# Optimization experiments

Hardware: AMD Instinct MI355X
Metric: run time of the kernel (lower is better)

## Reference

```python
import jax, jax.numpy as jnp
import numpy as np

EMBED = 1024
HEADS = 16
HEAD_DIM = EMBED // HEADS
LN_EPS = 1e-5


def setup_inputs() -> dict:
    key = jax.random.key(0)
    ks = jax.random.split(key, 7)
    B, S = 2, 2048
    x = jax.random.normal(ks[0], (B, S, EMBED), dtype=jnp.float32)
    attn_params = jax.random.uniform(ks[1], (B, S, 3 * EMBED), dtype=jnp.float32)
    sc = 1.0 / np.sqrt(EMBED)
    Wqkv = jax.random.normal(ks[2], (3 * EMBED, EMBED), dtype=jnp.float32) * sc
    Wout = jax.random.normal(ks[3], (EMBED, EMBED), dtype=jnp.float32) * sc
    b_out = jnp.zeros((EMBED,), dtype=jnp.float32)
    gamma = jnp.ones((EMBED,), dtype=jnp.float32)
    beta = jnp.zeros((EMBED,), dtype=jnp.float32)
    return {"x": x, "attn_params": attn_params, "Wqkv": Wqkv, "Wout": Wout,
            "b_out": b_out, "gamma": gamma, "beta": beta}


def reference(x, attn_params, Wqkv, Wout, b_out, gamma, beta):
    B, S, E = x.shape
    # qkv projection (no bias) followed by elementwise attn_params scaling
    qkv = jnp.einsum('bse,fe->bsf', x, Wqkv) * attn_params  # [B,S,3E]
    q, k, v = jnp.split(qkv, 3, axis=-1)
    # [B,H,S,D]
    q = q.reshape(B, S, HEADS, HEAD_DIM).transpose(0, 2, 1, 3)
    k = k.reshape(B, S, HEADS, HEAD_DIM).transpose(0, 2, 1, 3)
    v = v.reshape(B, S, HEADS, HEAD_DIM).transpose(0, 2, 1, 3)
    scores = jnp.einsum('bhqd,bhkd->bhqk', q, k) / jnp.sqrt(jnp.float32(HEAD_DIM))
    attn = jax.nn.softmax(scores, axis=-1)
    weighted = jnp.einsum('bhqk,bhkd->bhqd', attn, v)  # [B,H,S,D]
    weighted = weighted.transpose(0, 2, 1, 3).reshape(B, S, E)
    out = jnp.einsum('bse,fe->bsf', weighted, Wout) + b_out
    out = out + x  # residual
    # layernorm over last dim
    mu = jnp.mean(out, axis=-1, keepdims=True)
    var = jnp.mean(jnp.square(out - mu), axis=-1, keepdims=True)
    return (out - mu) * jax.lax.rsqrt(var + LN_EPS) * gamma + beta
```

## Files before the change

### kernel.cpp

```cpp
#include <hip/hip_runtime.h>

typedef float f32x4 __attribute__((ext_vector_type(4)));
typedef short s16x8 __attribute__((ext_vector_type(8)));
typedef unsigned short u16;

#define AS1 __attribute__((address_space(1)))
#define AS3 __attribute__((address_space(3)))

__device__ __forceinline__ u16 f2bf(float f){
    union { float f; unsigned u; } v; v.f = f;
    unsigned r = v.u + 0x7FFFu + ((v.u >> 16) & 1u);
    return (u16)(r >> 16);
}

__device__ __forceinline__ void pswap(unsigned &A, unsigned &B){
    asm("v_permlane32_swap_b32 %0, %1\n\tv_permlane16_swap_b32 %0, %1" : "+v"(A), "+v"(B));
}
__device__ __forceinline__ unsigned cvtpk(float lo, float hi){
    unsigned w;
    asm("v_cvt_pk_bf16_f32 %0, %1, %2" : "=v"(w) : "v"(lo), "v"(hi));
    return w;
}

__global__ __launch_bounds__(256) void cvt3_bf16(
    const float* __restrict__ a, u16* __restrict__ da, int na,
    const float* __restrict__ b, u16* __restrict__ db, int nb,
    const float* __restrict__ c, u16* __restrict__ dc, int nc)
{
    int i = blockIdx.x * 256 + threadIdx.x;
    const float* s; u16* d; int off;
    if (i < na){ s = a; d = da; off = i; }
    else if (i < na + nb){ s = b; d = db; off = i - na; }
    else if (i < na + nb + nc){ s = c; d = dc; off = i - na - nb; }
    else return;
    float4 v = ((const float4*)s)[off];
    ushort4 o;
    o.x = f2bf(v.x); o.y = f2bf(v.y); o.z = f2bf(v.z); o.w = f2bf(v.w);
    ((ushort4*)d)[off] = o;
}

__global__ __launch_bounds__(256) void gemm128_qkv(
    const u16* __restrict__ A, const u16* __restrict__ Bw,
    int N, int K,
    const float* __restrict__ e0, u16* __restrict__ Cout)
{
    __shared__ u16 As[2][128 * 32];
    __shared__ u16 Bs[2][128 * 32];
    const int tid = threadIdx.x;
    const int w = tid >> 6, lane = tid & 63;
    const int g = lane >> 4, c = lane & 15;
    const int wr = w >> 1, wc = w & 1;

    const int bid = blockIdx.x;
    const int xcd = bid & 7, lin = bid >> 3;
    const int rowBase = (xcd * 4 + (lin & 3)) * 128;
    const int colBase = (lin >> 2) * 128;

    f32x4 acc[4][4] = {};

    auto STAGE = [&](int pb, int k0){
#pragma unroll
        for (int i = 0; i < 2; ++i){
            int o  = i * 4096 + tid * 16;
            int r  = o >> 6;
            int ce = (o & 63) >> 1;
            const u16* ga = A  + (size_t)(rowBase + r) * K + (k0 + ce);
            __builtin_amdgcn_global_load_lds((const AS1 void*)ga,
                (AS3 void*)((char*)As[pb] + i * 4096 + w * 1024), 16, 0, 0);
            const u16* gb = Bw + (size_t)(colBase + r) * K + (k0 + ce);
            __builtin_amdgcn_global_load_lds((const AS1 void*)gb,
                (AS3 void*)((char*)Bs[pb] + i * 4096 + w * 1024), 16, 0, 0);
        }
    };

    const int nt = K >> 5;
    STAGE(0, 0);
    __syncthreads();

    for (int t = 0; t < nt; ++t){
        const int cur = t & 1;
        if (t + 1 < nt) STAGE(cur ^ 1, (t + 1) * 32);

        s16x8 af[4], bfr[4];
#pragma unroll
        for (int m = 0; m < 4; ++m){
            int row = wr * 64 + m * 16 + c;
            af[m] = *(const s16x8*)((const char*)As[cur] + row * 64 + g * 16);
        }
#pragma unroll
        for (int n = 0; n < 4; ++n){
            int row = wc * 64 + n * 16 + c;
            bfr[n] = *(const s16x8*)((const char*)Bs[cur] + row * 64 + g * 16);
        }
#pragma unroll
        for (int m = 0; m < 4; ++m)
#pragma unroll
            for (int n = 0; n < 4; ++n)
                acc[m][n] = __builtin_amdgcn_mfma_f32_16x16x32_bf16(af[m], bfr[n], acc[m][n], 0, 0, 0);
        __syncthreads();
    }

#pragma unroll
    for (int m = 0; m < 4; ++m){
        const int rbase = rowBase + wr * 64 + m * 16 + g * 4;
        float ev[16];
#pragma unroll
        for (int n = 0; n < 4; ++n){
            const int cc = colBase + wc * 64 + n * 16 + c;
#pragma unroll
            for (int j = 0; j < 4; ++j)
                ev[n * 4 + j] = e0[(size_t)(rbase + j) * N + cc];
        }
#pragma unroll
        for (int n = 0; n < 4; ++n){
            const int cc = colBase + wc * 64 + n * 16 + c;
#pragma unroll
            for (int j = 0; j < 4; ++j){
                float apv = ev[n * 4 + j];
                if (cc < 1024) apv *= 0.18033688f;
                Cout[(size_t)(rbase + j) * N + cc] = f2bf(acc[m][n][j] * apv);
            }
        }
    }
}

__global__ __launch_bounds__(256) void gemm_bt(
    const u16* __restrict__ A, const u16* __restrict__ Bw,
    int M, int N, int K,
    const float* __restrict__ e0, const float* __restrict__ e1,
    float* __restrict__ Cout)
{
    __shared__ u16 As[2][128 * 32];
    __shared__ u16 Bs[2][128 * 32];
    const int tid = threadIdx.x;
    const int w = tid >> 6, lane = tid & 63;
    const int g = lane >> 4, c = lane & 15;
    const int wr = w >> 1, wc = w & 1;
    const int rowBase = blockIdx.y * 128;
    const int colBase = blockIdx.x * 128;

    f32x4 acc[4][4] = {};

    auto STAGE = [&](int pb, int k0){
#pragma unroll
        for (int i = 0; i < 2; ++i){
            int o  = i * 4096 + tid * 16;
            int r  = o >> 6;
            int ce = (o & 63) >> 1;
            const u16* ga = A  + (size_t)(rowBase + r) * K + (k0 + ce);
            __builtin_amdgcn_global_load_lds((const AS1 void*)ga,
                (AS3 void*)((char*)As[pb] + i * 4096 + w * 1024), 16, 0, 0);
            const u16* gb = Bw + (size_t)(colBase + r) * K + (k0 + ce);
            __builtin_amdgcn_global_load_lds((const AS1 void*)gb,
                (AS3 void*)((char*)Bs[pb] + i * 4096 + w * 1024), 16, 0, 0);
        }
    };

    const int nt = K >> 5;
    STAGE(0, 0);
    __syncthreads();

    for (int t = 0; t < nt; ++t){
        const int cur = t & 1;
        if (t + 1 < nt) STAGE(cur ^ 1, (t + 1) * 32);

        s16x8 af[4], bfr[4];
#pragma unroll
        for (int m = 0; m < 4; ++m){
            int row = wr * 64 + m * 16 + c;
            af[m] = *(const s16x8*)((const char*)As[cur] + row * 64 + g * 16);
        }
#pragma unroll
        for (int n = 0; n < 4; ++n){
            int row = wc * 64 + n * 16 + c;
            bfr[n] = *(const s16x8*)((const char*)Bs[cur] + row * 64 + g * 16);
        }
#pragma unroll
        for (int m = 0; m < 4; ++m)
#pragma unroll
            for (int n = 0; n < 4; ++n)
                acc[m][n] = __builtin_amdgcn_mfma_f32_16x16x32_bf16(af[m], bfr[n], acc[m][n], 0, 0, 0);
        __syncthreads();
    }

    float bcol[4];
#pragma unroll
    for (int n = 0; n < 4; ++n)
        bcol[n] = e0[colBase + wc * 64 + n * 16 + c];

#pragma unroll
    for (int m = 0; m < 4; ++m){
        const int rbase = rowBase + wr * 64 + m * 16 + g * 4;
        float ev[16];
#pragma unroll
        for (int n = 0; n < 4; ++n){
            const int cc = colBase + wc * 64 + n * 16 + c;
#pragma unroll
            for (int j = 0; j < 4; ++j)
                ev[n * 4 + j] = e1[(size_t)(rbase + j) * N + cc];
        }
#pragma unroll
        for (int n = 0; n < 4; ++n){
            const int cc = colBase + wc * 64 + n * 16 + c;
#pragma unroll
            for (int j = 0; j < 4; ++j)
                Cout[(size_t)(rbase + j) * N + cc] = acc[m][n][j] + bcol[n] + ev[n * 4 + j];
        }
    }
}

__global__ __launch_bounds__(256) void vtrans(const u16* __restrict__ qkv, u16* __restrict__ vt){
    __shared__ u16 t_[64 * 64];
    int bh = blockIdx.x; int b = bh >> 4; int h = bh & 15;
    int st = blockIdx.y;
    int tid = threadIdx.x;
#pragma unroll
    for (int i = 0; i < 2; ++i){
        int id = i * 256 + tid;
        int sr = id >> 3, c8 = id & 7;
        uint4 v = *(const uint4*)(qkv + (size_t)(b * 2048 + st * 64 + sr) * 3072 + 2048 + h * 64 + c8 * 8);
        *(uint4*)((char*)t_ + ((sr * 128 + c8 * 16) ^ ((sr & 7) << 4))) = v;
    }
    __syncthreads();
#pragma unroll
    for (int i = 0; i < 2; ++i){
        int id = i * 256 + tid;
        int d = id >> 3, s8 = (id & 7) * 8;
        u16 tmp[8];
#pragma unroll
        for (int jj = 0; jj < 8; ++jj){
            int s = s8 + jj;
            tmp[jj] = *(const u16*)((const char*)t_ + ((s * 128 + d * 2) ^ ((s & 7) << 4)));
        }
        *(uint4*)(vt + ((size_t)bh * 64 + d) * 2048 + st * 64 + s8) = *(uint4*)tmp;
    }
}

__global__ __launch_bounds__(512) void attn_k(const u16* __restrict__ qkv,
                                              const u16* __restrict__ vt,
                                              u16* __restrict__ o)
{
    __shared__ u16 Kl[2][64 * 64];
    __shared__ u16 Vl[2][64 * 64];
    int bh = blockIdx.x; int b = bh >> 4, h = bh & 15;
    int qt = blockIdx.y;
    int tid = threadIdx.x;
    int w = tid >> 6, lane = tid & 63, g = lane >> 4, c = lane & 15;

    const size_t qrow = (size_t)(b * 2048 + qt * 128 + w * 16 + c);
    s16x8 qf[2];
    qf[0] = *(const s16x8*)(qkv + qrow * 3072 + h * 64 + g * 8);
    qf[1] = *(const s16x8*)(qkv + qrow * 3072 + h * 64 + 32 + g * 8);

    const s16x8 ones8 = {16256, 16256, 16256, 16256, 16256, 16256, 16256, 16256};

    f32x4 oa[4] = {};
    f32x4 la = {};

    int kr = tid >> 3, c8 = tid & 7;
    const u16* kg = qkv + (size_t)(b * 2048 + kr) * 3072 + 1024 + h * 64 + c8 * 8;
    const u16* vg = vt + ((size_t)bh * 64 + kr) * 2048 + c8 * 8;
    const int so = (kr * 128 + c8 * 16) ^ ((kr & 7) << 4);

    uint4 ks = *(const uint4*)kg;
    uint4 vs = *(const uint4*)vg;
    *(uint4*)((char*)Kl[0] + so) = ks;
    *(uint4*)((char*)Vl[0] + so) = vs;
    __syncthreads();

    for (int t = 0; t < 32; ++t){
        const int cur = t & 1;
        if (t < 31){
            ks = *(const uint4*)(kg + (size_t)(t + 1) * 64 * 3072);
            vs = *(const uint4*)(vg + (t + 1) * 64);
        }

        f32x4 st[4];
        __builtin_amdgcn_s_setprio(1);
#pragma unroll
        for (int kt = 0; kt < 4; ++kt){
            int row = kt * 16 + c;
            s16x8 kf0 = *(const s16x8*)((const char*)Kl[cur] + ((row * 128 + g * 16) ^ ((row & 7) << 4)));
            s16x8 kf1 = *(const s16x8*)((const char*)Kl[cur] + ((row * 128 + 64 + g * 16) ^ ((row & 7) << 4)));
            f32x4 a = {};
            a = __builtin_amdgcn_mfma_f32_16x16x32_bf16(kf0, qf[0], a, 0, 0, 0);
            a = __builtin_amdgcn_mfma_f32_16x16x32_bf16(kf1, qf[1], a, 0, 0, 0);
            st[kt] = a;
        }
        __builtin_amdgcn_s_setprio(0);

        unsigned W[4][2];
#pragma unroll
        for (int kt = 0; kt < 4; ++kt){
            float p0 = __builtin_amdgcn_exp2f(st[kt][0]);
            float p1 = __builtin_amdgcn_exp2f(st[kt][1]);
            float p2 = __builtin_amdgcn_exp2f(st[kt][2]);
            float p3 = __builtin_amdgcn_exp2f(st[kt][3]);
            W[kt][0] = cvtpk(p0, p1);
            W[kt][1] = cvtpk(p2, p3);
        }

        __builtin_amdgcn_s_setprio(1);
#pragma unroll
        for (int kb = 0; kb < 2; ++kb){
            unsigned t0 = W[kb * 2][0], t2 = W[kb * 2 + 1][0];
            pswap(t0, t2);
            unsigned t1 = W[kb * 2][1], t3 = W[kb * 2 + 1][1];
            pswap(t1, t3);
            union { unsigned u[4]; s16x8 v; } pu;
            pu.u[0] = t0; pu.u[1] = t1; pu.u[2] = t2; pu.u[3] = t3;
#pragma unroll
            for (int dt = 0; dt < 4; ++dt){
                int vrow = dt * 16 + c;
                s16x8 vf = *(const s16x8*)((const char*)Vl[cur] + ((vrow * 128 + kb * 64 + g * 16) ^ ((vrow & 7) << 4)));
                oa[dt] = __builtin_amdgcn_mfma_f32_16x16x32_bf16(vf, pu.v, oa[dt], 0, 0, 0);
            }
            la = __builtin_amdgcn_mfma_f32_16x16x32_bf16(ones8, pu.v, la, 0, 0, 0);
        }
        __builtin_amdgcn_s_setprio(0);

        if (t < 31){
            *(uint4*)((char*)Kl[cur ^ 1] + so) = ks;
            *(uint4*)((char*)Vl[cur ^ 1] + so) = vs;
        }
        __syncthreads();
    }

    float inv = 1.0f / la[0];
#pragma unroll
    for (int dt = 0; dt < 4; ++dt){
        u16 t4[4];
#pragma unroll
        for (int j = 0; j < 4; ++j) t4[j] = f2bf(oa[dt][j] * inv);
        *(uint2*)(o + qrow * 1024 + h * 64 + dt * 16 + g * 4) = *(uint2*)t4;
    }
}

__global__ __launch_bounds__(256) void ln_k(const float* __restrict__ tmp,
                                            const float* __restrict__ gamma,
                                            const float* __restrict__ beta,
                                            float* __restrict__ out)
{
    int row = blockIdx.x;
    int tid = threadIdx.x;
    float4 v = ((const float4*)(tmp + (size_t)row * 1024))[tid];
    float s  = v.x + v.y + v.z + v.w;
    float ss = v.x * v.x + v.y * v.y + v.z * v.z + v.w * v.w;
    for (int m = 1; m < 64; m <<= 1){ s += __shfl_xor(s, m); ss += __shfl_xor(ss, m); }
    __shared__ float red[8];
    int w = tid >> 6;
    if ((tid & 63) == 0){ red[w * 2] = s; red[w * 2 + 1] = ss; }
    __syncthreads();
    s  = red[0] + red[2] + red[4] + red[6];
    ss = red[1] + red[3] + red[5] + red[7];
    float mu  = s * (1.f / 1024.f);
    float var = ss * (1.f / 1024.f) - mu * mu;
    float inv = rsqrtf(var + 1e-5f);
    float4 g4 = ((const float4*)gamma)[tid];
    float4 b4 = ((const float4*)beta)[tid];
    float4 r;
    r.x = (v.x - mu) * inv * g4.x + b4.x;
    r.y = (v.y - mu) * inv * g4.y + b4.y;
    r.z = (v.z - mu) * inv * g4.z + b4.z;
    r.w = (v.w - mu) * inv * g4.w + b4.w;
    ((float4*)(out + (size_t)row * 1024))[tid] = r;
}

extern "C" void kernel_launch(void* const* d_in, const int* in_sizes, int n_in,
                              void* d_out, int out_size, void* d_ws, size_t ws_size,
                              hipStream_t stream)
{
    const float* x     = (const float*)d_in[0];
    const float* ap    = (const float*)d_in[1];
    const float* wqkv  = (const float*)d_in[2];
    const float* wout  = (const float*)d_in[3];
    const float* bout  = (const float*)d_in[4];
    const float* gamma = (const float*)d_in[5];
    const float* beta  = (const float*)d_in[6];
    float* out = (float*)d_out;

    char* ws = (char*)d_ws;
    u16* xb    = (u16*)ws;  ws += (size_t)4096 * 1024 * 2;
    u16* wqkvb = (u16*)ws;  ws += (size_t)3072 * 1024 * 2;
    u16* woutb = (u16*)ws;  ws += (size_t)1024 * 1024 * 2;
    u16* qkvb  = (u16*)ws;  ws += (size_t)4096 * 3072 * 2;
    u16* vtb   = (u16*)ws;  ws += (size_t)32 * 64 * 2048 * 2;
    u16* attnb = (u16*)ws;  ws += (size_t)4096 * 1024 * 2;
    float* tmp = (float*)ws;

    const int na = 4096 * 1024 / 4, nb = 3072 * 1024 / 4, nc = 1024 * 1024 / 4;
    cvt3_bf16<<<(na + nb + nc + 255) / 256, 256, 0, stream>>>(x, xb, na, wqkv, wqkvb, nb, wout, woutb, nc);

    gemm128_qkv<<<768, 256, 0, stream>>>(xb, wqkvb, 3072, 1024, ap, qkvb);
    vtrans<<<dim3(32, 32), 256, 0, stream>>>(qkvb, vtb);
    attn_k<<<dim3(32, 16), 512, 0, stream>>>(qkvb, vtb, attnb);
    gemm_bt<<<dim3(8, 32), 256, 0, stream>>>(attnb, woutb, 4096, 1024, 1024, bout, x, tmp);
    ln_k<<<4096, 256, 0, stream>>>(tmp, gamma, beta, out);
}
```

Before: 141.9 us.

## Double attention KV tile to 128 keys and drop XCD-aware QKV GEMM block mapping

The attention kernel now stages 128 keys per iteration instead of 64 into doubled LDS buffers, halving the number of loop iterations and barriers. Each iteration computes eight score tiles and four PV k-blocks. Separately, the QKV GEMM switches from an XCD-swizzled 1D block index to a plain 2D grid. This raises LDS use and register pressure in the attention kernel and may lose the L2 locality the XCD mapping provided.

Result: no change. 141.9 us (+0.0%).

```diff
diff --git a/kernel.cpp b/kernel.cpp
--- a/kernel.cpp
+++ b/kernel.cpp
@@ -39,7 +39,7 @@
     ((ushort4*)d)[off] = o;
 }
 
-__global__ __launch_bounds__(256) void gemm128_qkv(
+__global__ __launch_bounds__(256) void gemm_qkv(
     const u16* __restrict__ A, const u16* __restrict__ Bw,
     int N, int K,
     const float* __restrict__ e0, u16* __restrict__ Cout)
@@ -50,11 +50,8 @@
     const int w = tid >> 6, lane = tid & 63;
     const int g = lane >> 4, c = lane & 15;
     const int wr = w >> 1, wc = w & 1;
-
-    const int bid = blockIdx.x;
-    const int xcd = bid & 7, lin = bid >> 3;
-    const int rowBase = (xcd * 4 + (lin & 3)) * 128;
-    const int colBase = (lin >> 2) * 128;
+    const int rowBase = blockIdx.y * 128;
+    const int colBase = blockIdx.x * 128;
 
     f32x4 acc[4][4] = {};
 
@@ -240,8 +237,8 @@
                                               const u16* __restrict__ vt,
                                               u16* __restrict__ o)
 {
-    __shared__ u16 Kl[2][64 * 64];
-    __shared__ u16 Vl[2][64 * 64];
+    __shared__ u16 Kl[2][128 * 64];
+    __shared__ u16 Vl[2][64 * 128];
     int bh = blockIdx.x; int b = bh >> 4, h = bh & 15;
     int qt = blockIdx.y;
     int tid = threadIdx.x;
@@ -259,26 +256,36 @@
 
     int kr = tid >> 3, c8 = tid & 7;
     const u16* kg = qkv + (size_t)(b * 2048 + kr) * 3072 + 1024 + h * 64 + c8 * 8;
-    const u16* vg = vt + ((size_t)bh * 64 + kr) * 2048 + c8 * 8;
-    const int so = (kr * 128 + c8 * 16) ^ ((kr & 7) << 4);
-
-    uint4 ks = *(const uint4*)kg;
-    uint4 vs = *(const uint4*)vg;
-    *(uint4*)((char*)Kl[0] + so) = ks;
-    *(uint4*)((char*)Vl[0] + so) = vs;
+    const int sk0 = (kr * 128 + c8 * 16) ^ ((kr & 7) << 4);
+    const int sk1 = sk0 + 64 * 128;
+    int dr = tid >> 3;
+    const u16* vg = vt + ((size_t)bh * 64 + dr) * 2048 + c8 * 8;
+    const int sv0 = (dr * 256 + c8 * 16) ^ ((dr & 7) << 4);
+    const int sv1 = sv0 + 128;
+
+    uint4 ks0 = *(const uint4*)kg;
+    uint4 ks1 = *(const uint4*)(kg + (size_t)64 * 3072);
+    uint4 vs0 = *(const uint4*)vg;
+    uint4 vs1 = *(const uint4*)(vg + 64);
+    *(uint4*)((char*)Kl[0] + sk0) = ks0;
+    *(uint4*)((char*)Kl[0] + sk1) = ks1;
+    *(uint4*)((char*)Vl[0] + sv0) = vs0;
+    *(uint4*)((char*)Vl[0] + sv1) = vs1;
     __syncthreads();
 
-    for (int t = 0; t < 32; ++t){
+    for (int t = 0; t < 16; ++t){
         const int cur = t & 1;
-        if (t < 31){
-            ks = *(const uint4*)(kg + (size_t)(t + 1) * 64 * 3072);
-            vs = *(const uint4*)(vg + (t + 1) * 64);
-        }
-
-        f32x4 st[4];
+        if (t < 15){
+            ks0 = *(const uint4*)(kg + (size_t)(t + 1) * 128 * 3072);
+            ks1 = *(const uint4*)(kg + (size_t)(t + 1) * 128 * 3072 + (size_t)64 * 3072);
+            vs0 = *(const uint4*)(vg + (t + 1) * 128);
+            vs1 = *(const uint4*)(vg + (t + 1) * 128 + 64);
+        }
+
+        f32x4 st[8];
         __builtin_amdgcn_s_setprio(1);
 #pragma unroll
-        for (int kt = 0; kt < 4; ++kt){
+        for (int kt = 0; kt < 8; ++kt){
             int row = kt * 16 + c;
             s16x8 kf0 = *(const s16x8*)((const char*)Kl[cur] + ((row * 128 + g * 16) ^ ((row & 7) << 4)));
             s16x8 kf1 = *(const s16x8*)((const char*)Kl[cur] + ((row * 128 + 64 + g * 16) ^ ((row & 7) << 4)));
@@ -289,9 +296,9 @@
         }
         __builtin_amdgcn_s_setprio(0);
 
-        unsigned W[4][2];
-#pragma unroll
-        for (int kt = 0; kt < 4; ++kt){
+        unsigned W[8][2];
+#pragma unroll
+        for (int kt = 0; kt < 8; ++kt){
             float p0 = __builtin_amdgcn_exp2f(st[kt][0]);
             float p1 = __builtin_amdgcn_exp2f(st[kt][1]);
             float p2 = __builtin_amdgcn_exp2f(st[kt][2]);
@@ -302,7 +309,7 @@
 
         __builtin_amdgcn_s_setprio(1);
 #pragma unroll
-        for (int kb = 0; kb < 2; ++kb){
+        for (int kb = 0; kb < 4; ++kb){
             unsigned t0 = W[kb * 2][0], t2 = W[kb * 2 + 1][0];
             pswap(t0, t2);
             unsigned t1 = W[kb * 2][1], t3 = W[kb * 2 + 1][1];
@@ -312,16 +319,18 @@
 #pragma unroll
             for (int dt = 0; dt < 4; ++dt){
                 int vrow = dt * 16 + c;
-                s16x8 vf = *(const s16x8*)((const char*)Vl[cur] + ((vrow * 128 + kb * 64 + g * 16) ^ ((vrow & 7) << 4)));
+                s16x8 vf = *(const s16x8*)((const char*)Vl[cur] + ((vrow * 256 + kb * 64 + g * 16) ^ ((vrow & 7) << 4)));
                 oa[dt] = __builtin_amdgcn_mfma_f32_16x16x32_bf16(vf, pu.v, oa[dt], 0, 0, 0);
             }
             la = __builtin_amdgcn_mfma_f32_16x16x32_bf16(ones8, pu.v, la, 0, 0, 0);
         }
         __builtin_amdgcn_s_setprio(0);
 
-        if (t < 31){
-            *(uint4*)((char*)Kl[cur ^ 1] + so) = ks;
-            *(uint4*)((char*)Vl[cur ^ 1] + so) = vs;
+        if (t < 15){
+            *(uint4*)((char*)Kl[cur ^ 1] + sk0) = ks0;
+            *(uint4*)((char*)Kl[cur ^ 1] + sk1) = ks1;
+            *(uint4*)((char*)Vl[cur ^ 1] + sv0) = vs0;
+            *(uint4*)((char*)Vl[cur ^ 1] + sv1) = vs1;
         }
         __syncthreads();
     }
@@ -391,7 +400,7 @@
     const int na = 4096 * 1024 / 4, nb = 3072 * 1024 / 4, nc = 1024 * 1024 / 4;
     cvt3_bf16<<<(na + nb + nc + 255) / 256, 256, 0, stream>>>(x, xb, na, wqkv, wqkvb, nb, wout, woutb, nc);
 
-    gemm128_qkv<<<768, 256, 0, stream>>>(xb, wqkvb, 3072, 1024, ap, qkvb);
+    gemm_qkv<<<dim3(24, 32), 256, 0, stream>>>(xb, wqkvb, 3072, 1024, ap, qkvb);
     vtrans<<<dim3(32, 32), 256, 0, stream>>>(qkvb, vtb);
     attn_k<<<dim3(32, 16), 512, 0, stream>>>(qkvb, vtb, attnb);
     gemm_bt<<<dim3(8, 32), 256, 0, stream>>>(attnb, woutb, 4096, 1024, 1024, bout, x, tmp);
```
